# Kernel tuning notes

Hardware: AMD Instinct MI355X
Metric: run time of the kernel (lower is better)

The kernel has to match this reference:

```python
import jax, jax.numpy as jnp
import numpy as np

B = 32768          # number of independent 22-node graphs (batched block-diagonal)
G = 22             # nodes per graph (22 players; 22*5 = 110 = readout in_features)
N = B * G          # total nodes
E = N * G          # complete digraph with self-loops per graph: 22*22 edges/graph


def setup_inputs() -> dict:
    key = jax.random.key(0)
    ks = jax.random.split(key, 9)
    features = jax.random.normal(ks[0], (N, 9), jnp.float32)
    # block-diagonal complete digraph (with self-loops) per 22-node graph
    offsets = np.repeat(np.arange(B, dtype=np.int32) * G, G * G)
    local_src = np.tile(np.repeat(np.arange(G, dtype=np.int32), G), B)
    local_dst = np.tile(np.tile(np.arange(G, dtype=np.int32), G), B)
    src = jnp.asarray(offsets + local_src)
    dst = jnp.asarray(offsets + local_dst)

    def lin(k, fan_in, fan_out):
        bound = 1.0 / np.sqrt(fan_in)
        kw, kb = jax.random.split(k)
        W = jax.random.uniform(kw, (fan_in, fan_out), jnp.float32, -bound, bound)
        b = jax.random.uniform(kb, (fan_out,), jnp.float32, -bound, bound)
        return W, b

    W_lift, b_lift = lin(ks[1], 9, 15)
    W1, b1 = lin(ks[2], 15, 10)
    W2, b2 = lin(ks[3], 10, 5)
    W_ro, b_ro = lin(ks[4], 110, 1)
    return dict(features=features, src=src, dst=dst,
                W_lift=W_lift, b_lift=b_lift, W1=W1, b1=b1,
                W2=W2, b2=b2, W_ro=W_ro, b_ro=b_ro)


def _gcn(x, src, dst, W, b):
    # DGL copy_src + sum: gather source features per edge, scatter-sum into dst,
    # then linear + relu node update.
    agg = jax.ops.segment_sum(x[src], dst, num_segments=N)
    return jax.nn.relu(agg @ W + b)


def reference(features, src, dst, W_lift, b_lift, W1, b1, W2, b2, W_ro, b_ro):
    x = jax.nn.relu(features @ W_lift + b_lift)   # [N, 15]
    x = _gcn(x, src, dst, W1, b1)                 # [N, 10]
    x = _gcn(x, src, dst, W2, b2)                 # [N, 5]
    x = x.reshape(B, G * 5)                       # [B, 110]
    # dropout is identity in eval mode
    return x @ W_ro + b_ro                        # [B, 1]
```

## Files before the change

### kernel.cpp

```cpp
#include <hip/hip_runtime.h>


typedef float v2f __attribute__((ext_vector_type(2)));

#define G_NODES 22
#define PPG     11
#define GPB     11
#define ACT     (GPB*PPG)
#define BLK     128
#define FIN     9
#define LF      15
#define NP      8
#define H1      10
#define H2      5
#define SPAD    17

__global__ __launch_bounds__(BLK) void gnn_fused(
    const float* __restrict__ feat,
    const float* __restrict__ Wl, const float* __restrict__ bl,
    const float* __restrict__ W1, const float* __restrict__ b1,
    const float* __restrict__ W2, const float* __restrict__ b2,
    const float* __restrict__ Wro, const float* __restrict__ bro,
    float* __restrict__ out, int nGraphs)
{
    __shared__ float sP[ACT * SPAD];

    const int t = threadIdx.x;
    const int g = t / PPG;
    const long gg = (long)blockIdx.x * GPB + g;
    const bool act = (t < ACT) && (gg < (long)nGraphs);

    if (act) {
        const float2* f2 = (const float2*)feat + ((long)blockIdx.x * ACT + t) * FIN;
        float fv[2 * FIN];
        #pragma unroll
        for (int j = 0; j < FIN; ++j) {
            const float2 v = f2[j];
            fv[2 * j] = v.x; fv[2 * j + 1] = v.y;
        }

        v2f a2[NP], c2[NP];
        #pragma unroll
        for (int i = 0; i < NP; ++i) {
            const float blo = bl[2 * i];
            const float bhi = (2 * i + 1 < LF) ? bl[2 * i + 1] : 0.0f;
            a2[i] = (v2f){blo, bhi};
            c2[i] = (v2f){blo, bhi};
        }
        #pragma unroll
        for (int j = 0; j < FIN; ++j) {
            const v2f f0 = (v2f){fv[j], fv[j]};
            const v2f f1 = (v2f){fv[FIN + j], fv[FIN + j]};
            #pragma unroll
            for (int i = 0; i < NP; ++i) {
                const v2f w = (v2f){Wl[j * LF + 2 * i],
                                    (2 * i + 1 < LF) ? Wl[j * LF + 2 * i + 1]
                                                     : 0.0f};
                a2[i] += f0 * w;
                c2[i] += f1 * w;
            }
        }
        #pragma unroll
        for (int i = 0; i < NP; ++i) {
            sP[t * SPAD + 2 * i] =
                fmaxf(a2[i].x, 0.0f) + fmaxf(c2[i].x, 0.0f);
            if (2 * i + 1 < LF)
                sP[t * SPAD + 2 * i + 1] =
                    fmaxf(a2[i].y, 0.0f) + fmaxf(c2[i].y, 0.0f);
        }
    }
    __syncthreads();

    if (t < GPB) {
        const long gg2 = (long)blockIdx.x * GPB + t;
        if (gg2 < (long)nGraphs) {
            float S[LF];
            #pragma unroll
            for (int k = 0; k < LF; ++k) S[k] = 0.0f;
            #pragma unroll
            for (int n = 0; n < PPG; ++n)
                #pragma unroll
                for (int k = 0; k < LF; ++k)
                    S[k] += sP[(t * PPG + n) * SPAD + k];

            float x1[H1];
            #pragma unroll
            for (int k = 0; k < H1; ++k) {
                float v = b1[k];
                #pragma unroll
                for (int j = 0; j < LF; ++j)
                    v = fmaf(S[j], W1[j * H1 + k], v);
                x1[k] = fmaxf(v, 0.0f) * (float)G_NODES;
            }

            float x2[H2];
            #pragma unroll
            for (int k = 0; k < H2; ++k) {
                float v = b2[k];
                #pragma unroll
                for (int j = 0; j < H1; ++j)
                    v = fmaf(x1[j], W2[j * H2 + k], v);
                x2[k] = fmaxf(v, 0.0f);
            }

            float o = bro[0];
            #pragma unroll
            for (int k = 0; k < H2; ++k) {
                float wc = 0.0f;
                #pragma unroll
                for (int m = 0; m < G_NODES; ++m)
                    wc += Wro[m * H2 + k];
                o = fmaf(x2[k], wc, o);
            }
            out[gg2] = o;
        }
    }
}

extern "C" void kernel_launch(void* const* d_in, const int* in_sizes, int n_in,
                              void* d_out, int out_size, void* d_ws, size_t ws_size,
                              hipStream_t stream) {
    const float* feat = (const float*)d_in[0];
    const float* Wl  = (const float*)d_in[3];
    const float* bl  = (const float*)d_in[4];
    const float* W1  = (const float*)d_in[5];
    const float* b1  = (const float*)d_in[6];
    const float* W2  = (const float*)d_in[7];
    const float* b2  = (const float*)d_in[8];
    const float* Wro = (const float*)d_in[9];
    const float* bro = (const float*)d_in[10];
    float* out = (float*)d_out;

    const int B    = in_sizes[0] / (G_NODES * FIN);
    const int grid = (B + GPB - 1) / GPB;

    gnn_fused<<<grid, BLK, 0, stream>>>(feat, Wl, bl, W1, b1, W2, b2, Wro, bro,
                                        out, B);
}
```

Baseline: 13.28 us.

## Load features as float4 with four nodes per thread, 32 graphs per block

Each thread now reads 9 float4s, which covers four nodes (two adjacent node pairs), instead of 9 float2s. The per-pair relu sums are combined in registers and written to shared memory in a new layout of 6 rows per graph, with the thread whose pairs cross a graph boundary writing two rows. Blocks grow to 192 threads and handle 32 graphs, so there are fewer blocks and wider memory transactions. The cost is more register pressure, fewer reader threads per block, and a clamp on the load index for the tail block.

```diff
diff --git a/kernel.cpp b/kernel.cpp
--- a/kernel.cpp
+++ b/kernel.cpp
@@ -4,15 +4,18 @@
 typedef float v2f __attribute__((ext_vector_type(2)));
 
 #define G_NODES 22
-#define PPG     11
-#define GPB     11
-#define ACT     (GPB*PPG)
-#define BLK     128
 #define FIN     9
 #define LF      15
 #define NP      8
 #define H1      10
 #define H2      5
+#define GRP     11
+#define NGRP    16
+#define GPB     (2*NGRP)
+#define ACT     (NGRP*GRP)
+#define BLK     192
+#define PPGRAPH 6
+#define ROWS    (GPB*PPGRAPH)
 #define SPAD    17
 
 __global__ __launch_bounds__(BLK) void gnn_fused(
@@ -21,67 +24,93 @@
     const float* __restrict__ W1, const float* __restrict__ b1,
     const float* __restrict__ W2, const float* __restrict__ b2,
     const float* __restrict__ Wro, const float* __restrict__ bro,
-    float* __restrict__ out, int nGraphs)
+    float* __restrict__ out, int nGraphs, long totF4)
 {
-    __shared__ float sP[ACT * SPAD];
+    __shared__ float sP[ROWS * SPAD];
 
     const int t = threadIdx.x;
-    const int g = t / PPG;
-    const long gg = (long)blockIdx.x * GPB + g;
-    const bool act = (t < ACT) && (gg < (long)nGraphs);
 
-    if (act) {
-        const float2* f2 = (const float2*)feat + ((long)blockIdx.x * ACT + t) * FIN;
-        float fv[2 * FIN];
+    if (t < ACT) {
+        const int gi = t / GRP;
+        const int u  = t - gi * GRP;
+        long f4idx = (long)blockIdx.x * (GPB * G_NODES * FIN / 4) + 9L * t;
+        if (f4idx > totF4 - 9) f4idx = totF4 - 9;
+        const float4* f4 = (const float4*)feat;
+
+        float fv[36];
         #pragma unroll
-        for (int j = 0; j < FIN; ++j) {
-            const float2 v = f2[j];
-            fv[2 * j] = v.x; fv[2 * j + 1] = v.y;
+        for (int j = 0; j < 9; ++j) {
+            const float4 q = f4[f4idx + j];
+            fv[4*j+0] = q.x; fv[4*j+1] = q.y; fv[4*j+2] = q.z; fv[4*j+3] = q.w;
         }
 
-        v2f a2[NP], c2[NP];
+        v2f sum[2][NP];
         #pragma unroll
-        for (int i = 0; i < NP; ++i) {
-            const float blo = bl[2 * i];
-            const float bhi = (2 * i + 1 < LF) ? bl[2 * i + 1] : 0.0f;
-            a2[i] = (v2f){blo, bhi};
-            c2[i] = (v2f){blo, bhi};
-        }
-        #pragma unroll
-        for (int j = 0; j < FIN; ++j) {
-            const v2f f0 = (v2f){fv[j], fv[j]};
-            const v2f f1 = (v2f){fv[FIN + j], fv[FIN + j]};
+        for (int h = 0; h < 2; ++h) {
+            v2f a2[NP], c2[NP];
             #pragma unroll
             for (int i = 0; i < NP; ++i) {
-                const v2f w = (v2f){Wl[j * LF + 2 * i],
-                                    (2 * i + 1 < LF) ? Wl[j * LF + 2 * i + 1]
-                                                     : 0.0f};
-                a2[i] += f0 * w;
-                c2[i] += f1 * w;
+                const float blo = bl[2*i];
+                const float bhi = (2*i+1 < LF) ? bl[2*i+1] : 0.0f;
+                a2[i] = (v2f){blo, bhi};
+                c2[i] = (v2f){blo, bhi};
+            }
+            #pragma unroll
+            for (int j = 0; j < FIN; ++j) {
+                const v2f f0 = (v2f){fv[h*18 + j],       fv[h*18 + j]};
+                const v2f f1 = (v2f){fv[h*18 + FIN + j], fv[h*18 + FIN + j]};
+                #pragma unroll
+                for (int i = 0; i < NP; ++i) {
+                    const v2f w = (v2f){Wl[j*LF + 2*i],
+                                        (2*i+1 < LF) ? Wl[j*LF + 2*i+1] : 0.0f};
+                    a2[i] += f0 * w;
+                    c2[i] += f1 * w;
+                }
+            }
+            #pragma unroll
+            for (int i = 0; i < NP; ++i) {
+                sum[h][i].x = fmaxf(a2[i].x, 0.0f) + fmaxf(c2[i].x, 0.0f);
+                sum[h][i].y = fmaxf(a2[i].y, 0.0f) + fmaxf(c2[i].y, 0.0f);
             }
         }
-        #pragma unroll
-        for (int i = 0; i < NP; ++i) {
-            sP[t * SPAD + 2 * i] =
-                fmaxf(a2[i].x, 0.0f) + fmaxf(c2[i].x, 0.0f);
-            if (2 * i + 1 < LF)
-                sP[t * SPAD + 2 * i + 1] =
-                    fmaxf(a2[i].y, 0.0f) + fmaxf(c2[i].y, 0.0f);
+
+        const int g0 = 2*gi, g1 = 2*gi + 1;
+        if (u == 5) {
+            const int rA = (g0*PPGRAPH + 5) * SPAD;
+            const int rB = (g1*PPGRAPH + 0) * SPAD;
+            #pragma unroll
+            for (int i = 0; i < NP; ++i) {
+                sP[rA + 2*i] = sum[0][i].x;
+                sP[rB + 2*i] = sum[1][i].x;
+                if (2*i+1 < LF) {
+                    sP[rA + 2*i+1] = sum[0][i].y;
+                    sP[rB + 2*i+1] = sum[1][i].y;
+                }
+            }
+        } else {
+            const int row = (u < 5) ? (g0*PPGRAPH + u) : (g1*PPGRAPH + (u - 5));
+            const int r = row * SPAD;
+            #pragma unroll
+            for (int i = 0; i < NP; ++i) {
+                sP[r + 2*i] = sum[0][i].x + sum[1][i].x;
+                if (2*i+1 < LF)
+                    sP[r + 2*i+1] = sum[0][i].y + sum[1][i].y;
+            }
         }
     }
     __syncthreads();
 
     if (t < GPB) {
-        const long gg2 = (long)blockIdx.x * GPB + t;
-        if (gg2 < (long)nGraphs) {
+        const long gg = (long)blockIdx.x * GPB + t;
+        if (gg < (long)nGraphs) {
             float S[LF];
             #pragma unroll
             for (int k = 0; k < LF; ++k) S[k] = 0.0f;
             #pragma unroll
-            for (int n = 0; n < PPG; ++n)
+            for (int n = 0; n < PPGRAPH; ++n)
                 #pragma unroll
                 for (int k = 0; k < LF; ++k)
-                    S[k] += sP[(t * PPG + n) * SPAD + k];
+                    S[k] += sP[(t*PPGRAPH + n) * SPAD + k];
 
             float x1[H1];
             #pragma unroll
@@ -89,7 +118,7 @@
                 float v = b1[k];
                 #pragma unroll
                 for (int j = 0; j < LF; ++j)
-                    v = fmaf(S[j], W1[j * H1 + k], v);
+                    v = fmaf(S[j], W1[j*H1 + k], v);
                 x1[k] = fmaxf(v, 0.0f) * (float)G_NODES;
             }
 
@@ -99,7 +128,7 @@
                 float v = b2[k];
                 #pragma unroll
                 for (int j = 0; j < H1; ++j)
-                    v = fmaf(x1[j], W2[j * H2 + k], v);
+                    v = fmaf(x1[j], W2[j*H2 + k], v);
                 x2[k] = fmaxf(v, 0.0f);
             }
 
@@ -109,10 +138,10 @@
                 float wc = 0.0f;
                 #pragma unroll
                 for (int m = 0; m < G_NODES; ++m)
-                    wc += Wro[m * H2 + k];
+                    wc += Wro[m*H2 + k];
                 o = fmaf(x2[k], wc, o);
             }
-            out[gg2] = o;
+            out[gg] = o;
         }
     }
 }
@@ -131,9 +160,10 @@
     const float* bro = (const float*)d_in[10];
     float* out = (float*)d_out;
 
-    const int B    = in_sizes[0] / (G_NODES * FIN);
-    const int grid = (B + GPB - 1) / GPB;
+    const int  B     = in_sizes[0] / (G_NODES * FIN);
+    const long totF4 = (long)in_sizes[0] / 4;
+    const int  grid  = (B + GPB - 1) / GPB;
 
     gnn_fused<<<grid, BLK, 0, stream>>>(feat, Wl, bl, W1, b1, W2, b2, Wro, bro,
-                                        out, B);
+                                        out, B, totF4);
 }
```

New measurement: 12.75 us. 4.0% less time.
